# Kernel tuning notes

Hardware: AMD Instinct MI355X
Metric: run time of the kernel (lower is better)

## Reference

```python
import jax, jax.numpy as jnp
import numpy as np

B = 4
IMAGE = 64
SAMPLES = 24
LATENT = 128
HIDDEN = 128
CAMERA_D = 2.0
NEAR, FAR = CAMERA_D - 1.0, CAMERA_D + 1.0
FOV_T = float(np.tan(np.arcsin(1.0 / CAMERA_D)))  # frustum tangent to unit sphere
SHARPNESS = 50.0


def _view_field():
    # canonical per-pixel ray directions, camera looking down -z
    c = ((np.arange(IMAGE) + 0.5) / IMAGE * 2.0 - 1.0) * FOV_T
    xx, yy = np.meshgrid(c, -c, indexing='xy')  # [H, W]
    d = np.stack([xx, yy, -np.ones_like(xx)], axis=-1)
    d /= np.linalg.norm(d, axis=-1, keepdims=True)
    return d.astype(np.float32)  # [H, W, 3]


def _frustum_mask_idx():
    # static mask: pixels whose canonical ray intersects the unit sphere
    d = _view_field().reshape(-1, 3)
    o = np.array([0.0, 0.0, CAMERA_D])
    disc = (d @ o) ** 2 - (o @ o - 1.0)
    return np.nonzero(disc >= 0.0)[0].astype(np.int32)


def setup_inputs() -> dict:
    key = jax.random.key(0)
    k = jax.random.split(key, 8)

    def w(ki, shape):
        return jax.random.normal(ki, shape, jnp.float32) * np.sqrt(2.0 / shape[0])

    return {
        'latents': jax.random.normal(k[0], (B, LATENT), jnp.float32) * 0.01,
        'phis': jax.random.uniform(k[1], (B,), jnp.float32) * (np.pi / 3.0),
        'thetas': jax.random.uniform(k[2], (B,), jnp.float32) * (2.0 * np.pi),
        'samples_u': jax.random.uniform(k[3], (IMAGE, IMAGE, SAMPLES), jnp.float32),
        'w1': w(k[4], (3 + LATENT, HIDDEN)), 'b1': jnp.zeros((HIDDEN,), jnp.float32),
        'w2': w(k[5], (HIDDEN, HIDDEN)), 'b2': jnp.zeros((HIDDEN,), jnp.float32),
        'w_sdf': w(k[6], (HIDDEN, 1)), 'b_sdf': jnp.zeros((1,), jnp.float32),
        'w_tex': w(k[7], (HIDDEN, 3)), 'b_tex': jnp.zeros((3,), jnp.float32),
    }


def reference(latents, phis, thetas, samples_u, w1, b1, w2, b2, w_sdf, b_sdf, w_tex, b_tex):
    mask_idx = jnp.asarray(_frustum_mask_idx())  # [R] static
    n_rays = int(mask_idx.shape[0])
    d_cam = jnp.asarray(_view_field())  # [H, W, 3]

    def feats(P, Z):  # latent-conditioned SDF MLP trunk
        h = jax.nn.relu(jnp.concatenate([P, Z], -1) @ w1 + b1)
        return jax.nn.relu(h @ w2 + b2)

    def sdf_val(P, Z):
        return (feats(P, Z) @ w_sdf + b_sdf)[..., 0]

    # sphereToRect: camera position on sphere of radius CAMERA_D
    cp, sp = jnp.cos(phis), jnp.sin(phis)
    ct, st = jnp.cos(thetas), jnp.sin(thetas)
    cam_loc = CAMERA_D * jnp.stack([cp * st, sp, cp * ct], -1)  # [B, 3]

    # enumerateRays: rotate canonical view field to look at the origin
    f = -cam_loc / jnp.linalg.norm(cam_loc, axis=-1, keepdims=True)
    up0 = jnp.broadcast_to(jnp.array([0.0, 1.0, 0.0], jnp.float32), f.shape)
    right = jnp.cross(up0, f)
    right = right / jnp.linalg.norm(right, axis=-1, keepdims=True)
    up = jnp.cross(f, right)
    R = jnp.stack([right, up, -f], axis=-1)  # [B, 3, 3], columns = camera axes
    rays = jnp.einsum('bij,hwj->bhwi', R, d_cam).reshape(B, IMAGE * IMAGE, 3)
    rays_m = rays[:, mask_idx]  # [B, R, 3]

    # sampleStratified: per-pixel jittered depths in [NEAR, FAR]
    bins = (jnp.arange(SAMPLES, dtype=jnp.float32) + samples_u) * ((FAR - NEAR) / SAMPLES) + NEAR
    samples_m = bins.reshape(IMAGE * IMAGE, SAMPLES)[mask_idx]  # [R, S]

    # scaleRays: world-space sample points per ray
    targets = cam_loc[:, None, None, :] + rays_m[:, :, None, :] * samples_m[None, :, :, None]  # [B,R,S,3]

    # fastRayIntegral: SDF at all samples, pick first sub-zero crossing per ray
    Z_all = jnp.broadcast_to(latents[:, None, :], (B, n_rays * SAMPLES, LATENT)).reshape(-1, LATENT)
    vals = sdf_val(targets.reshape(-1, 3), Z_all).reshape(B, n_rays, SAMPLES)
    below = vals <= 0.0
    idx = jnp.where(below.any(-1), jnp.argmax(below, -1), jnp.argmin(vals, -1))  # [B, R]
    hit = jnp.take_along_axis(targets, idx[:, :, None, None], axis=2)[:, :, 0]  # [B, R, 3]
    Ph = hit.reshape(-1, 3)
    Zh = jnp.broadcast_to(latents[:, None, :], (B, n_rays, LATENT)).reshape(-1, LATENT)
    values, vjp = jax.vjp(lambda P: sdf_val(P, Zh), Ph)
    normals, = vjp(jnp.ones_like(values))  # SDF spatial gradient = surface normal
    texture = jax.nn.sigmoid(feats(Ph, Zh) @ w_tex + b_tex)  # [B*R, 3]

    # shade: Lambertian with soft hit weight, then masked scatter into the image
    light = jnp.array([1.0, 1.0, 1.0], jnp.float32) / np.sqrt(3.0)
    n_hat = normals / (jnp.linalg.norm(normals, axis=-1, keepdims=True) + 1e-8)
    lambert = jnp.clip(n_hat @ light, 0.0, 1.0)
    hit_w = jax.nn.sigmoid(-values * SHARPNESS)
    shaded = (texture * ((0.2 + 0.8 * lambert) * hit_w)[:, None]).reshape(B, n_rays, 3)
    result = jnp.zeros((B, IMAGE * IMAGE, 3), shaded.dtype).at[:, mask_idx].set(shaded)
    return result.reshape(B, IMAGE, IMAGE, 3).transpose(0, 3, 1, 2)  # [B, 3, H, W]
```

## Files before the change

### kernel.cpp

```cpp
#include <hip/hip_runtime.h>
#include <math.h>

typedef short bf16x8 __attribute__((ext_vector_type(8)));
typedef float f32x4 __attribute__((ext_vector_type(4)));

#define BATCH 4
#define IMG 64
#define NSAMP 24
#define HID 128
#define LATN 128
#define PIX 8
#define MPT (PIX*NSAMP)
#define FOV_T 0.57735026918962576f
#define CAMD 2.0f
#define NEARP 1.0f
#define STEP (2.0f/24.0f)
#define SHARP 50.0f

#define WS_LAT1 0
#define WS_CAMR 512
#define WS_W2T  1024
#define WS_L1P  17408
#define WS_W2S  19456

__device__ __forceinline__ unsigned short f2bf(float f) {
    unsigned int u = __float_as_uint(f);
    u = u + 0x7FFFu + ((u >> 16) & 1u);
    return (unsigned short)(u >> 16);
}
__device__ __forceinline__ float bf2f(unsigned short s) {
    return __uint_as_float(((unsigned int)s) << 16);
}

__global__ void setup_batch(const float* __restrict__ latents,
                            const float* __restrict__ phis,
                            const float* __restrict__ thetas,
                            const float* __restrict__ w1,
                            const float* __restrict__ b1,
                            float* __restrict__ ws) {
    int b = blockIdx.x, j = threadIdx.x;
    float acc = b1[j];
    for (int k = 0; k < LATN; ++k)
        acc = fmaf(latents[b*LATN + k], w1[(3+k)*HID + j], acc);
    ws[WS_LAT1 + b*HID + j] = acc;
    float4 pk = make_float4(w1[j], w1[HID + j], w1[2*HID + j], acc);
    *(float4*)&ws[WS_L1P + (b*HID + j)*4] = pk;
    if (j == 0) {
        float ph = phis[b], th = thetas[b];
        float cp = cosf(ph), sp = sinf(ph), ct = cosf(th), st = sinf(th);
        float cx = CAMD*cp*st, cy = CAMD*sp, cz = CAMD*cp*ct;
        float nc = sqrtf(cx*cx + cy*cy + cz*cz);
        float fx = -cx/nc, fy = -cy/nc, fz = -cz/nc;
        float rx = fz, rz = -fx;
        float nr = sqrtf(rx*rx + rz*rz);
        rx /= nr; rz /= nr;
        float ux = fy*rz;
        float uy = fz*rx - fx*rz;
        float uz = -fy*rx;
        float* c = ws + WS_CAMR + b*12;
        c[0]=cx; c[1]=cy; c[2]=cz;
        c[3]=rx; c[4]=0.0f; c[5]=rz;
        c[6]=ux; c[7]=uy; c[8]=uz;
        c[9]=fx; c[10]=fy; c[11]=fz;
    }
}

__global__ void setup_w2t(const float* __restrict__ w2, float* __restrict__ ws) {
    int j = blockIdx.x, k = threadIdx.x;
    ws[WS_W2T + j*HID + k] = w2[k*HID + j];
}

__global__ void setup_w2s(const float* __restrict__ w2, unsigned short* __restrict__ w2s) {
    int id = blockIdx.x*256 + threadIdx.x;
    int k0 = id >> 9, n0 = (id >> 6) & 7, l = id & 63;
    int n = n0*16 + (l & 15);
    #pragma unroll
    for (int i = 0; i < 8; ++i) {
        int k = k0*32 + (l >> 4)*8 + i;
        float w = w2[k*HID + n];
        unsigned short u0 = f2bf(w);   float f0 = bf2f(u0);
        float r1 = w - f0;  unsigned short u1 = f2bf(r1); float f1 = bf2f(u1);
        float r2 = r1 - f1; unsigned short u2 = f2bf(r2);
        int base = ((k0*8 + n0)*64 + l)*8 + i;
        w2s[base]         = u0;
        w2s[16384 + base] = u1;
        w2s[32768 + base] = u2;
    }
}

__global__ __launch_bounds__(256, 2)
void render_kernel(const float* __restrict__ samples_u,
                   const float* __restrict__ w1,
                   const float* __restrict__ w2,
                   const float* __restrict__ b2,
                   const float* __restrict__ w_sdf,
                   const float* __restrict__ b_sdf,
                   const float* __restrict__ w_tex,
                   const float* __restrict__ b_tex,
                   const float* __restrict__ ws,
                   float* __restrict__ out) {
    __shared__ __align__(16) float4 Ps4[MPT];
    __shared__ __align__(16) float4 l1ps[HID];
    __shared__ float vals[MPT];
    __shared__ float b2s[HID];
    __shared__ float wsds[HID];
    __shared__ float shadeH[4*HID];
    __shared__ float shadeD[4*HID];
    __shared__ float lat1s[HID];
    __shared__ float camR[12];
    __shared__ int   hitMs[PIX];
    __shared__ int   maskq[PIX];

    const int t    = threadIdx.x;
    const int lane = t & 63;
    const int wv   = __builtin_amdgcn_readfirstlane(t >> 6);
    const int blk  = blockIdx.x;
    const int b    = blk >> 9;
    const int tile = blk & 511;

    if (t < 12)  camR[t]  = ws[WS_CAMR + b*12 + t];
    if (t < HID) {
        lat1s[t] = ws[WS_LAT1 + b*HID + t];
        l1ps[t]  = ((const float4*)(ws + WS_L1P))[b*HID + t];
        b2s[t]   = b2[t];
        wsds[t]  = w_sdf[t];
    }
    if (t < PIX) {
        int p = tile*PIX + t;
        int x = p & 63, y = p >> 6;
        float xx = ((x + 0.5f)*(2.0f/IMG) - 1.0f)*FOV_T;
        float yy = ((y + 0.5f)*(2.0f/IMG) - 1.0f)*FOV_T;
        float n2 = xx*xx + yy*yy + 1.0f;
        maskq[t] = (4.0f - 3.0f*n2) >= 0.0f ? 1 : 0;
    }
    __syncthreads();

    {
        int any = maskq[0]|maskq[1]|maskq[2]|maskq[3]|maskq[4]|maskq[5]|maskq[6]|maskq[7];
        if (!any) {
            if (t < PIX*3) {
                int q = t & 7, ch = t >> 3;
                int p = tile*PIX + q;
                int x = p & 63, y = p >> 6;
                out[((b*3 + ch)*IMG + y)*IMG + x] = 0.0f;
            }
            return;
        }
    }

    if (t < MPT) {
        int q = t / NSAMP, s = t - q*NSAMP;
        int p = tile*PIX + q;
        int x = p & 63, y = p >> 6;
        float xx =  ((x + 0.5f)*(2.0f/IMG) - 1.0f)*FOV_T;
        float yy = -(((y + 0.5f)*(2.0f/IMG) - 1.0f)*FOV_T);
        float inv = 1.0f/sqrtf(xx*xx + yy*yy + 1.0f);
        float d0 = xx*inv, d1 = yy*inv, d2 = -inv;
        float rxv = camR[3]*d0 + camR[6]*d1 - camR[9]*d2;
        float ryv = camR[4]*d0 + camR[7]*d1 - camR[10]*d2;
        float rzv = camR[5]*d0 + camR[8]*d1 - camR[11]*d2;
        float u  = samples_u[(y*IMG + x)*NSAMP + s];
        float tv = (s + u)*STEP + NEARP;
        Ps4[t] = make_float4(fmaf(rxv, tv, camR[0]),
                             fmaf(ryv, tv, camR[1]),
                             fmaf(rzv, tv, camR[2]), 0.0f);
    }
    __syncthreads();

    {
        const unsigned short* w2s = (const unsigned short*)(ws + WS_W2S);
        const int lm = lane & 15, lg = lane >> 4;
        const float bsdf = b_sdf[0];

        float4 Pm0 = Ps4[(wv*3+0)*16 + lm];
        float4 Pm1 = Ps4[(wv*3+1)*16 + lm];
        float4 Pm2 = Ps4[(wv*3+2)*16 + lm];

        f32x4 acc[3][8];
        #pragma unroll
        for (int mt = 0; mt < 3; ++mt)
            #pragma unroll
            for (int n0 = 0; n0 < 8; ++n0)
                acc[mt][n0] = (f32x4)(0.0f);

        for (int k0 = 0; k0 < 4; ++k0) {
            bf16x8 a0[3], a1[3], a2[3];
            #pragma unroll
            for (int mt = 0; mt < 3; ++mt) {
                float4 P = (mt == 0) ? Pm0 : ((mt == 1) ? Pm1 : Pm2);
                #pragma unroll
                for (int i = 0; i < 8; ++i) {
                    float4 wl = l1ps[k0*32 + lg*8 + i];
                    float h = fmaxf(fmaf(P.x, wl.x, fmaf(P.y, wl.y, fmaf(P.z, wl.z, wl.w))), 0.0f);
                    unsigned short u0 = f2bf(h);  float f0 = bf2f(u0);
                    float r1 = h - f0;  unsigned short u1 = f2bf(r1); float f1 = bf2f(u1);
                    float r2 = r1 - f1; unsigned short u2 = f2bf(r2);
                    a0[mt][i] = (short)u0; a1[mt][i] = (short)u1; a2[mt][i] = (short)u2;
                }
            }
            const unsigned short* wk = w2s + (k0*8)*512 + lane*8;
            #pragma unroll
            for (int n0 = 0; n0 < 8; ++n0) {
                bf16x8 B0 = *(const bf16x8*)(wk + n0*512);
                bf16x8 B1 = *(const bf16x8*)(wk + 16384 + n0*512);
                bf16x8 B2 = *(const bf16x8*)(wk + 32768 + n0*512);
                #pragma unroll
                for (int mt = 0; mt < 3; ++mt) {
                    f32x4 c = acc[mt][n0];
                    c = __builtin_amdgcn_mfma_f32_16x16x32_bf16(a0[mt], B0, c, 0, 0, 0);
                    c = __builtin_amdgcn_mfma_f32_16x16x32_bf16(a0[mt], B1, c, 0, 0, 0);
                    c = __builtin_amdgcn_mfma_f32_16x16x32_bf16(a1[mt], B0, c, 0, 0, 0);
                    c = __builtin_amdgcn_mfma_f32_16x16x32_bf16(a0[mt], B2, c, 0, 0, 0);
                    c = __builtin_amdgcn_mfma_f32_16x16x32_bf16(a1[mt], B1, c, 0, 0, 0);
                    c = __builtin_amdgcn_mfma_f32_16x16x32_bf16(a2[mt], B0, c, 0, 0, 0);
                    acc[mt][n0] = c;
                }
            }
        }

        #pragma unroll
        for (int mt = 0; mt < 3; ++mt) {
            float ps0 = 0.0f, ps1 = 0.0f, ps2 = 0.0f, ps3 = 0.0f;
            #pragma unroll
            for (int n0 = 0; n0 < 8; ++n0) {
                int j = n0*16 + lm;
                float bb = b2s[j], wd = wsds[j];
                ps0 += fmaxf(acc[mt][n0][0] + bb, 0.0f)*wd;
                ps1 += fmaxf(acc[mt][n0][1] + bb, 0.0f)*wd;
                ps2 += fmaxf(acc[mt][n0][2] + bb, 0.0f)*wd;
                ps3 += fmaxf(acc[mt][n0][3] + bb, 0.0f)*wd;
            }
            #pragma unroll
            for (int off = 1; off < 16; off <<= 1) {
                ps0 += __shfl_xor(ps0, off, 64);
                ps1 += __shfl_xor(ps1, off, 64);
                ps2 += __shfl_xor(ps2, off, 64);
                ps3 += __shfl_xor(ps3, off, 64);
            }
            if (lm == 0) {
                int mg = (wv*3 + mt)*16 + lg*4;
                vals[mg+0] = ps0 + bsdf;
                vals[mg+1] = ps1 + bsdf;
                vals[mg+2] = ps2 + bsdf;
                vals[mg+3] = ps3 + bsdf;
            }
        }
    }
    __syncthreads();

    if (t < PIX) {
        int base = t*NSAMP;
        int idx = -1, bidx = 0;
        float bestv = 3.0e38f;
        for (int s = 0; s < NSAMP; ++s) {
            float v = vals[base + s];
            if (idx < 0 && v <= 0.0f) idx = s;
            if (v < bestv) { bestv = v; bidx = s; }
        }
        hitMs[t] = base + (idx >= 0 ? idx : bidx);
    }
    __syncthreads();

    const float* w2t = ws + WS_W2T;
    const int j0 = lane, j1 = lane + 64;

    for (int pp = 0; pp < 2; ++pp) {
        int pt = pp*4 + wv;
        int hm = hitMs[pt];
        float4 H = Ps4[hm];
        float hx = H.x, hy = H.y, hz = H.z;

        float z0 = fmaf(hx, w1[j0], fmaf(hy, w1[HID+j0], fmaf(hz, w1[2*HID+j0], lat1s[j0])));
        float z1 = fmaf(hx, w1[j1], fmaf(hy, w1[HID+j1], fmaf(hz, w1[2*HID+j1], lat1s[j1])));
        float h10 = fmaxf(z0, 0.0f), h11 = fmaxf(z1, 0.0f);
        shadeH[wv*HID + j0] = h10;
        shadeH[wv*HID + j1] = h11;

        float a00=0,a01=0,a02=0,a03=0, a10=0,a11=0,a12=0,a13=0;
        for (int k = 0; k < HID; k += 4) {
            float4 hv = *(const float4*)&shadeH[wv*HID + k];
            a00 = fmaf(hv.x, w2[(k+0)*HID + j0], a00);
            a10 = fmaf(hv.x, w2[(k+0)*HID + j1], a10);
            a01 = fmaf(hv.y, w2[(k+1)*HID + j0], a01);
            a11 = fmaf(hv.y, w2[(k+1)*HID + j1], a11);
            a02 = fmaf(hv.z, w2[(k+2)*HID + j0], a02);
            a12 = fmaf(hv.z, w2[(k+2)*HID + j1], a12);
            a03 = fmaf(hv.w, w2[(k+3)*HID + j0], a03);
            a13 = fmaf(hv.w, w2[(k+3)*HID + j1], a13);
        }
        float za = (a00+a01)+(a02+a03) + b2[j0];
        float zb = (a10+a11)+(a12+a13) + b2[j1];
        float h20 = fmaxf(za, 0.0f), h21 = fmaxf(zb, 0.0f);
        float wsd0 = w_sdf[j0], wsd1 = w_sdf[j1];
        shadeD[wv*HID + j0] = (za > 0.0f) ? wsd0 : 0.0f;
        shadeD[wv*HID + j1] = (zb > 0.0f) ? wsd1 : 0.0f;

        float pv = h20*wsd0 + h21*wsd1;
        float p0 = h20*w_tex[j0*3+0] + h21*w_tex[j1*3+0];
        float p1 = h20*w_tex[j0*3+1] + h21*w_tex[j1*3+1];
        float p2 = h20*w_tex[j0*3+2] + h21*w_tex[j1*3+2];
        #pragma unroll
        for (int off = 32; off > 0; off >>= 1) {
            pv += __shfl_xor(pv, off, 64);
            p0 += __shfl_xor(p0, off, 64);
            p1 += __shfl_xor(p1, off, 64);
            p2 += __shfl_xor(p2, off, 64);
        }

        float d00=0,d01=0,d02=0,d03=0, d10=0,d11=0,d12=0,d13=0;
        for (int k = 0; k < HID; k += 4) {
            float4 dv = *(const float4*)&shadeD[wv*HID + k];
            d00 = fmaf(dv.x, w2t[(k+0)*HID + j0], d00);
            d10 = fmaf(dv.x, w2t[(k+0)*HID + j1], d10);
            d01 = fmaf(dv.y, w2t[(k+1)*HID + j0], d01);
            d11 = fmaf(dv.y, w2t[(k+1)*HID + j1], d11);
            d02 = fmaf(dv.z, w2t[(k+2)*HID + j0], d02);
            d12 = fmaf(dv.z, w2t[(k+2)*HID + j1], d12);
            d03 = fmaf(dv.w, w2t[(k+3)*HID + j0], d03);
            d13 = fmaf(dv.w, w2t[(k+3)*HID + j1], d13);
        }
        float dh0 = (d00+d01)+(d02+d03);
        float dh1v = (d10+d11)+(d12+d13);
        float dz10 = (h10 > 0.0f) ? dh0 : 0.0f;
        float dz11 = (h11 > 0.0f) ? dh1v : 0.0f;
        float g0 = w1[j0]*dz10 + w1[j1]*dz11;
        float g1 = w1[HID+j0]*dz10 + w1[HID+j1]*dz11;
        float g2 = w1[2*HID+j0]*dz10 + w1[2*HID+j1]*dz11;
        #pragma unroll
        for (int off = 32; off > 0; off >>= 1) {
            g0 += __shfl_xor(g0, off, 64);
            g1 += __shfl_xor(g1, off, 64);
            g2 += __shfl_xor(g2, off, 64);
        }

        if (lane == 0) {
            float val = pv + b_sdf[0];
            float nn = sqrtf(g0*g0 + g1*g1 + g2*g2) + 1e-8f;
            const float is3 = 0.57735026918962576f;
            float lam = (g0 + g1 + g2)*is3/nn;
            lam = fminf(fmaxf(lam, 0.0f), 1.0f);
            float hw = 1.0f/(1.0f + expf(val*SHARP));
            float sh = (0.2f + 0.8f*lam)*hw;
            int p = tile*PIX + pt;
            int x = p & 63, y = p >> 6;
            float o0 = 0.0f, o1 = 0.0f, o2 = 0.0f;
            if (maskq[pt]) {
                o0 = sh/(1.0f + expf(-(p0 + b_tex[0])));
                o1 = sh/(1.0f + expf(-(p1 + b_tex[1])));
                o2 = sh/(1.0f + expf(-(p2 + b_tex[2])));
            }
            out[((b*3 + 0)*IMG + y)*IMG + x] = o0;
            out[((b*3 + 1)*IMG + y)*IMG + x] = o1;
            out[((b*3 + 2)*IMG + y)*IMG + x] = o2;
        }
    }
}

extern "C" void kernel_launch(void* const* d_in, const int* in_sizes, int n_in,
                              void* d_out, int out_size, void* d_ws, size_t ws_size,
                              hipStream_t stream) {
    const float* latents   = (const float*)d_in[0];
    const float* phis      = (const float*)d_in[1];
    const float* thetas    = (const float*)d_in[2];
    const float* samples_u = (const float*)d_in[3];
    const float* w1        = (const float*)d_in[4];
    const float* b1        = (const float*)d_in[5];
    const float* w2        = (const float*)d_in[6];
    const float* b2        = (const float*)d_in[7];
    const float* w_sdf     = (const float*)d_in[8];
    const float* b_sdf     = (const float*)d_in[9];
    const float* w_tex     = (const float*)d_in[10];
    const float* b_tex     = (const float*)d_in[11];
    float* out = (float*)d_out;
    float* ws  = (float*)d_ws;

    setup_batch<<<dim3(BATCH), dim3(HID), 0, stream>>>(latents, phis, thetas, w1, b1, ws);
    setup_w2t<<<dim3(HID), dim3(HID), 0, stream>>>(w2, ws);
    setup_w2s<<<dim3(8), dim3(256), 0, stream>>>(w2, (unsigned short*)(ws + WS_W2S));
    render_kernel<<<dim3(BATCH*(IMG*IMG/PIX)), dim3(256), 0, stream>>>(
        samples_u, w1, w2, b2, w_sdf, b_sdf, w_tex, b_tex, ws, out);
}
```

Baseline: 218.7 us.

## Batch hit-point shading across 8 pixels and merge setup kernels into one

The per-wave shading loop, which handled one pixel at a time with two hidden units per lane, becomes a block-wide pass. All 8 hit points go through layer 2 and its backward pass together, with each thread owning one hidden unit across 4 pixels, so each w2 weight load is reused four times. Partial sums are reduced through small shared arrays and finished by 8 threads. The three setup kernels are fused into one launch to cut launch overhead. The cost is extra barriers and shared memory, plus a serial epilogue on a few threads.

```diff
diff --git a/kernel.cpp b/kernel.cpp
--- a/kernel.cpp
+++ b/kernel.cpp
@@ -32,59 +32,63 @@
     return __uint_as_float(((unsigned int)s) << 16);
 }
 
-__global__ void setup_batch(const float* __restrict__ latents,
-                            const float* __restrict__ phis,
-                            const float* __restrict__ thetas,
-                            const float* __restrict__ w1,
-                            const float* __restrict__ b1,
-                            float* __restrict__ ws) {
-    int b = blockIdx.x, j = threadIdx.x;
-    float acc = b1[j];
-    for (int k = 0; k < LATN; ++k)
-        acc = fmaf(latents[b*LATN + k], w1[(3+k)*HID + j], acc);
-    ws[WS_LAT1 + b*HID + j] = acc;
-    float4 pk = make_float4(w1[j], w1[HID + j], w1[2*HID + j], acc);
-    *(float4*)&ws[WS_L1P + (b*HID + j)*4] = pk;
-    if (j == 0) {
-        float ph = phis[b], th = thetas[b];
-        float cp = cosf(ph), sp = sinf(ph), ct = cosf(th), st = sinf(th);
-        float cx = CAMD*cp*st, cy = CAMD*sp, cz = CAMD*cp*ct;
-        float nc = sqrtf(cx*cx + cy*cy + cz*cz);
-        float fx = -cx/nc, fy = -cy/nc, fz = -cz/nc;
-        float rx = fz, rz = -fx;
-        float nr = sqrtf(rx*rx + rz*rz);
-        rx /= nr; rz /= nr;
-        float ux = fy*rz;
-        float uy = fz*rx - fx*rz;
-        float uz = -fy*rx;
-        float* c = ws + WS_CAMR + b*12;
-        c[0]=cx; c[1]=cy; c[2]=cz;
-        c[3]=rx; c[4]=0.0f; c[5]=rz;
-        c[6]=ux; c[7]=uy; c[8]=uz;
-        c[9]=fx; c[10]=fy; c[11]=fz;
-    }
-}
-
-__global__ void setup_w2t(const float* __restrict__ w2, float* __restrict__ ws) {
-    int j = blockIdx.x, k = threadIdx.x;
-    ws[WS_W2T + j*HID + k] = w2[k*HID + j];
-}
-
-__global__ void setup_w2s(const float* __restrict__ w2, unsigned short* __restrict__ w2s) {
-    int id = blockIdx.x*256 + threadIdx.x;
-    int k0 = id >> 9, n0 = (id >> 6) & 7, l = id & 63;
-    int n = n0*16 + (l & 15);
-    #pragma unroll
-    for (int i = 0; i < 8; ++i) {
-        int k = k0*32 + (l >> 4)*8 + i;
-        float w = w2[k*HID + n];
-        unsigned short u0 = f2bf(w);   float f0 = bf2f(u0);
-        float r1 = w - f0;  unsigned short u1 = f2bf(r1); float f1 = bf2f(u1);
-        float r2 = r1 - f1; unsigned short u2 = f2bf(r2);
-        int base = ((k0*8 + n0)*64 + l)*8 + i;
-        w2s[base]         = u0;
-        w2s[16384 + base] = u1;
-        w2s[32768 + base] = u2;
+__global__ void setup_all(const float* __restrict__ latents,
+                          const float* __restrict__ phis,
+                          const float* __restrict__ thetas,
+                          const float* __restrict__ w1,
+                          const float* __restrict__ b1,
+                          const float* __restrict__ w2,
+                          float* __restrict__ ws) {
+    const int bid = blockIdx.x, t = threadIdx.x;
+    if (bid < 4) {
+        if (t < HID) {
+            int b = bid, j = t;
+            float acc = b1[j];
+            for (int k = 0; k < LATN; ++k)
+                acc = fmaf(latents[b*LATN + k], w1[(3+k)*HID + j], acc);
+            ws[WS_LAT1 + b*HID + j] = acc;
+            float4 pk = make_float4(w1[j], w1[HID + j], w1[2*HID + j], acc);
+            *(float4*)&ws[WS_L1P + (b*HID + j)*4] = pk;
+            if (j == 0) {
+                float ph = phis[b], th = thetas[b];
+                float cp = cosf(ph), sp = sinf(ph), ct = cosf(th), st = sinf(th);
+                float cx = CAMD*cp*st, cy = CAMD*sp, cz = CAMD*cp*ct;
+                float nc = sqrtf(cx*cx + cy*cy + cz*cz);
+                float fx = -cx/nc, fy = -cy/nc, fz = -cz/nc;
+                float rx = fz, rz = -fx;
+                float nr = sqrtf(rx*rx + rz*rz);
+                rx /= nr; rz /= nr;
+                float ux = fy*rz;
+                float uy = fz*rx - fx*rz;
+                float uz = -fy*rx;
+                float* c = ws + WS_CAMR + b*12;
+                c[0]=cx; c[1]=cy; c[2]=cz;
+                c[3]=rx; c[4]=0.0f; c[5]=rz;
+                c[6]=ux; c[7]=uy; c[8]=uz;
+                c[9]=fx; c[10]=fy; c[11]=fz;
+            }
+        }
+    } else if (bid < 68) {
+        int id = (bid - 4)*256 + t;
+        int j = id >> 7, k = id & 127;
+        ws[WS_W2T + j*HID + k] = w2[k*HID + j];
+    } else {
+        int id = (bid - 68)*256 + t;
+        unsigned short* w2s = (unsigned short*)(ws + WS_W2S);
+        int k0 = id >> 9, n0 = (id >> 6) & 7, l = id & 63;
+        int n = n0*16 + (l & 15);
+        #pragma unroll
+        for (int i = 0; i < 8; ++i) {
+            int k = k0*32 + (l >> 4)*8 + i;
+            float w = w2[k*HID + n];
+            unsigned short u0 = f2bf(w);   float f0 = bf2f(u0);
+            float r1 = w - f0;  unsigned short u1 = f2bf(r1); float f1 = bf2f(u1);
+            float r2 = r1 - f1; unsigned short u2 = f2bf(r2);
+            int base = ((k0*8 + n0)*64 + l)*8 + i;
+            w2s[base]         = u0;
+            w2s[16384 + base] = u1;
+            w2s[32768 + base] = u2;
+        }
     }
 }
 
@@ -101,13 +105,15 @@
                    float* __restrict__ out) {
     __shared__ __align__(16) float4 Ps4[MPT];
     __shared__ __align__(16) float4 l1ps[HID];
+    __shared__ __align__(16) float4 shadeHT[HID*2];
+    __shared__ __align__(16) float4 dz2s[HID*2];
     __shared__ float vals[MPT];
     __shared__ float b2s[HID];
     __shared__ float wsds[HID];
-    __shared__ float shadeH[4*HID];
-    __shared__ float shadeD[4*HID];
     __shared__ float lat1s[HID];
     __shared__ float camR[12];
+    __shared__ float redp[4][16];
+    __shared__ float redg[4][12];
     __shared__ int   hitMs[PIX];
     __shared__ int   maskq[PIX];
 
@@ -239,10 +245,10 @@
             }
             if (lm == 0) {
                 int mg = (wv*3 + mt)*16 + lg*4;
-                vals[mg+0] = ps0 + bsdf;
-                vals[mg+1] = ps1 + bsdf;
-                vals[mg+2] = ps2 + bsdf;
-                vals[mg+3] = ps3 + bsdf;
+                vals[mg+0] = ps0 + b_sdf[0];
+                vals[mg+1] = ps1 + b_sdf[0];
+                vals[mg+2] = ps2 + b_sdf[0];
+                vals[mg+3] = ps3 + b_sdf[0];
             }
         }
     }
@@ -261,98 +267,132 @@
     }
     __syncthreads();
 
-    const float* w2t = ws + WS_W2T;
-    const int j0 = lane, j1 = lane + 64;
-
-    for (int pp = 0; pp < 2; ++pp) {
-        int pt = pp*4 + wv;
-        int hm = hitMs[pt];
-        float4 H = Ps4[hm];
-        float hx = H.x, hy = H.y, hz = H.z;
-
-        float z0 = fmaf(hx, w1[j0], fmaf(hy, w1[HID+j0], fmaf(hz, w1[2*HID+j0], lat1s[j0])));
-        float z1 = fmaf(hx, w1[j1], fmaf(hy, w1[HID+j1], fmaf(hz, w1[2*HID+j1], lat1s[j1])));
-        float h10 = fmaxf(z0, 0.0f), h11 = fmaxf(z1, 0.0f);
-        shadeH[wv*HID + j0] = h10;
-        shadeH[wv*HID + j1] = h11;
-
-        float a00=0,a01=0,a02=0,a03=0, a10=0,a11=0,a12=0,a13=0;
-        for (int k = 0; k < HID; k += 4) {
-            float4 hv = *(const float4*)&shadeH[wv*HID + k];
-            a00 = fmaf(hv.x, w2[(k+0)*HID + j0], a00);
-            a10 = fmaf(hv.x, w2[(k+0)*HID + j1], a10);
-            a01 = fmaf(hv.y, w2[(k+1)*HID + j0], a01);
-            a11 = fmaf(hv.y, w2[(k+1)*HID + j1], a11);
-            a02 = fmaf(hv.z, w2[(k+2)*HID + j0], a02);
-            a12 = fmaf(hv.z, w2[(k+2)*HID + j1], a12);
-            a03 = fmaf(hv.w, w2[(k+3)*HID + j0], a03);
-            a13 = fmaf(hv.w, w2[(k+3)*HID + j1], a13);
-        }
-        float za = (a00+a01)+(a02+a03) + b2[j0];
-        float zb = (a10+a11)+(a12+a13) + b2[j1];
-        float h20 = fmaxf(za, 0.0f), h21 = fmaxf(zb, 0.0f);
-        float wsd0 = w_sdf[j0], wsd1 = w_sdf[j1];
-        shadeD[wv*HID + j0] = (za > 0.0f) ? wsd0 : 0.0f;
-        shadeD[wv*HID + j1] = (zb > 0.0f) ? wsd1 : 0.0f;
-
-        float pv = h20*wsd0 + h21*wsd1;
-        float p0 = h20*w_tex[j0*3+0] + h21*w_tex[j1*3+0];
-        float p1 = h20*w_tex[j0*3+1] + h21*w_tex[j1*3+1];
-        float p2 = h20*w_tex[j0*3+2] + h21*w_tex[j1*3+2];
-        #pragma unroll
-        for (int off = 32; off > 0; off >>= 1) {
-            pv += __shfl_xor(pv, off, 64);
-            p0 += __shfl_xor(p0, off, 64);
-            p1 += __shfl_xor(p1, off, 64);
-            p2 += __shfl_xor(p2, off, 64);
-        }
-
-        float d00=0,d01=0,d02=0,d03=0, d10=0,d11=0,d12=0,d13=0;
-        for (int k = 0; k < HID; k += 4) {
-            float4 dv = *(const float4*)&shadeD[wv*HID + k];
-            d00 = fmaf(dv.x, w2t[(k+0)*HID + j0], d00);
-            d10 = fmaf(dv.x, w2t[(k+0)*HID + j1], d10);
-            d01 = fmaf(dv.y, w2t[(k+1)*HID + j0], d01);
-            d11 = fmaf(dv.y, w2t[(k+1)*HID + j1], d11);
-            d02 = fmaf(dv.z, w2t[(k+2)*HID + j0], d02);
-            d12 = fmaf(dv.z, w2t[(k+2)*HID + j1], d12);
-            d03 = fmaf(dv.w, w2t[(k+3)*HID + j0], d03);
-            d13 = fmaf(dv.w, w2t[(k+3)*HID + j1], d13);
-        }
-        float dh0 = (d00+d01)+(d02+d03);
-        float dh1v = (d10+d11)+(d12+d13);
-        float dz10 = (h10 > 0.0f) ? dh0 : 0.0f;
-        float dz11 = (h11 > 0.0f) ? dh1v : 0.0f;
-        float g0 = w1[j0]*dz10 + w1[j1]*dz11;
-        float g1 = w1[HID+j0]*dz10 + w1[HID+j1]*dz11;
-        float g2 = w1[2*HID+j0]*dz10 + w1[2*HID+j1]*dz11;
-        #pragma unroll
-        for (int off = 32; off > 0; off >>= 1) {
-            g0 += __shfl_xor(g0, off, 64);
-            g1 += __shfl_xor(g1, off, 64);
-            g2 += __shfl_xor(g2, off, 64);
-        }
-
-        if (lane == 0) {
-            float val = pv + b_sdf[0];
-            float nn = sqrtf(g0*g0 + g1*g1 + g2*g2) + 1e-8f;
-            const float is3 = 0.57735026918962576f;
-            float lam = (g0 + g1 + g2)*is3/nn;
-            lam = fminf(fmaxf(lam, 0.0f), 1.0f);
-            float hw = 1.0f/(1.0f + expf(val*SHARP));
-            float sh = (0.2f + 0.8f*lam)*hw;
-            int p = tile*PIX + pt;
-            int x = p & 63, y = p >> 6;
-            float o0 = 0.0f, o1 = 0.0f, o2 = 0.0f;
-            if (maskq[pt]) {
-                o0 = sh/(1.0f + expf(-(p0 + b_tex[0])));
-                o1 = sh/(1.0f + expf(-(p1 + b_tex[1])));
-                o2 = sh/(1.0f + expf(-(p2 + b_tex[2])));
-            }
-            out[((b*3 + 0)*IMG + y)*IMG + x] = o0;
-            out[((b*3 + 1)*IMG + y)*IMG + x] = o1;
-            out[((b*3 + 2)*IMG + y)*IMG + x] = o2;
-        }
+
+    #pragma unroll
+    for (int i = 0; i < 4; ++i) {
+        int idx = i*256 + t;
+        int p = idx & 7, k = idx >> 3;
+        float4 wl = l1ps[k];
+        float4 P  = Ps4[hitMs[p]];
+        float h = fmaxf(fmaf(P.x, wl.x, fmaf(P.y, wl.y, fmaf(P.z, wl.z, wl.w))), 0.0f);
+        ((float*)shadeHT)[k*8 + p] = h;
+    }
+    __syncthreads();
+
+    {
+        const int j = t & 127, ph = t >> 7;
+        float ac0 = 0.0f, ac1 = 0.0f, ac2 = 0.0f, ac3 = 0.0f;
+        const float* w2col = w2 + j;
+        #pragma unroll 8
+        for (int k = 0; k < HID; ++k) {
+            float wv2 = w2col[k*HID];
+            float4 hk = shadeHT[k*2 + ph];
+            ac0 = fmaf(hk.x, wv2, ac0);
+            ac1 = fmaf(hk.y, wv2, ac1);
+            ac2 = fmaf(hk.z, wv2, ac2);
+            ac3 = fmaf(hk.w, wv2, ac3);
+        }
+        float b2j = b2s[j], wsdj = wsds[j];
+        float tx0 = w_tex[j*3+0], tx1 = w_tex[j*3+1], tx2 = w_tex[j*3+2];
+        float z[4] = {ac0 + b2j, ac1 + b2j, ac2 + b2j, ac3 + b2j};
+        float4 dzv;
+        float vp[4], tp0[4], tp1[4], tp2[4];
+        #pragma unroll
+        for (int pp = 0; pp < 4; ++pp) {
+            float h2 = fmaxf(z[pp], 0.0f);
+            ((float*)&dzv)[pp] = (z[pp] > 0.0f) ? wsdj : 0.0f;
+            vp[pp]  = h2*wsdj;
+            tp0[pp] = h2*tx0;
+            tp1[pp] = h2*tx1;
+            tp2[pp] = h2*tx2;
+        }
+        dz2s[j*2 + ph] = dzv;
+        #pragma unroll
+        for (int pp = 0; pp < 4; ++pp) {
+            float v = vp[pp], a = tp0[pp], bt = tp1[pp], c = tp2[pp];
+            #pragma unroll
+            for (int off = 32; off > 0; off >>= 1) {
+                v  += __shfl_xor(v,  off, 64);
+                a  += __shfl_xor(a,  off, 64);
+                bt += __shfl_xor(bt, off, 64);
+                c  += __shfl_xor(c,  off, 64);
+            }
+            if (lane == 0) {
+                redp[wv][pp*4+0] = v;
+                redp[wv][pp*4+1] = a;
+                redp[wv][pp*4+2] = bt;
+                redp[wv][pp*4+3] = c;
+            }
+        }
+    }
+    __syncthreads();
+
+    {
+        const int k = t & 127, ph = t >> 7;
+        float d0 = 0.0f, d1 = 0.0f, d2 = 0.0f, d3 = 0.0f;
+        const float* wtcol = ws + WS_W2T + k;
+        #pragma unroll 8
+        for (int j = 0; j < HID; ++j) {
+            float wt = wtcol[j*HID];
+            float4 dz = dz2s[j*2 + ph];
+            d0 = fmaf(dz.x, wt, d0);
+            d1 = fmaf(dz.y, wt, d1);
+            d2 = fmaf(dz.z, wt, d2);
+            d3 = fmaf(dz.w, wt, d3);
+        }
+        float4 hh = shadeHT[k*2 + ph];
+        float4 wl = l1ps[k];
+        float dzl[4] = { (hh.x > 0.0f) ? d0 : 0.0f,
+                         (hh.y > 0.0f) ? d1 : 0.0f,
+                         (hh.z > 0.0f) ? d2 : 0.0f,
+                         (hh.w > 0.0f) ? d3 : 0.0f };
+        #pragma unroll
+        for (int pp = 0; pp < 4; ++pp) {
+            float g0 = wl.x*dzl[pp];
+            float g1 = wl.y*dzl[pp];
+            float g2 = wl.z*dzl[pp];
+            #pragma unroll
+            for (int off = 32; off > 0; off >>= 1) {
+                g0 += __shfl_xor(g0, off, 64);
+                g1 += __shfl_xor(g1, off, 64);
+                g2 += __shfl_xor(g2, off, 64);
+            }
+            if (lane == 0) {
+                redg[wv][0*4+pp] = g0;
+                redg[wv][1*4+pp] = g1;
+                redg[wv][2*4+pp] = g2;
+            }
+        }
+    }
+    __syncthreads();
+
+    if (t < PIX) {
+        int p = t, pp = p & 3;
+        int wA = (p < 4) ? 0 : 2;
+        float val  = redp[wA][pp*4+0] + redp[wA+1][pp*4+0] + b_sdf[0];
+        float tex0 = redp[wA][pp*4+1] + redp[wA+1][pp*4+1] + b_tex[0];
+        float tex1 = redp[wA][pp*4+2] + redp[wA+1][pp*4+2] + b_tex[1];
+        float tex2 = redp[wA][pp*4+3] + redp[wA+1][pp*4+3] + b_tex[2];
+        float g0 = redg[wA][0*4+pp] + redg[wA+1][0*4+pp];
+        float g1 = redg[wA][1*4+pp] + redg[wA+1][1*4+pp];
+        float g2 = redg[wA][2*4+pp] + redg[wA+1][2*4+pp];
+        float nn = sqrtf(g0*g0 + g1*g1 + g2*g2) + 1e-8f;
+        const float is3 = 0.57735026918962576f;
+        float lam = (g0 + g1 + g2)*is3/nn;
+        lam = fminf(fmaxf(lam, 0.0f), 1.0f);
+        float hw = 1.0f/(1.0f + expf(val*SHARP));
+        float sh = (0.2f + 0.8f*lam)*hw;
+        int pg = tile*PIX + p;
+        int x = pg & 63, y = pg >> 6;
+        float o0 = 0.0f, o1 = 0.0f, o2 = 0.0f;
+        if (maskq[p]) {
+            o0 = sh/(1.0f + expf(-tex0));
+            o1 = sh/(1.0f + expf(-tex1));
+            o2 = sh/(1.0f + expf(-tex2));
+        }
+        out[((b*3 + 0)*IMG + y)*IMG + x] = o0;
+        out[((b*3 + 1)*IMG + y)*IMG + x] = o1;
+        out[((b*3 + 2)*IMG + y)*IMG + x] = o2;
     }
 }
 
@@ -374,9 +414,7 @@
     float* out = (float*)d_out;
     float* ws  = (float*)d_ws;
 
-    setup_batch<<<dim3(BATCH), dim3(HID), 0, stream>>>(latents, phis, thetas, w1, b1, ws);
-    setup_w2t<<<dim3(HID), dim3(HID), 0, stream>>>(w2, ws);
-    setup_w2s<<<dim3(8), dim3(256), 0, stream>>>(w2, (unsigned short*)(ws + WS_W2S));
+    setup_all<<<dim3(76), dim3(256), 0, stream>>>(latents, phis, thetas, w1, b1, w2, ws);
     render_kernel<<<dim3(BATCH*(IMG*IMG/PIX)), dim3(256), 0, stream>>>(
         samples_u, w1, w2, b2, w_sdf, b_sdf, w_tex, b_tex, ws, out);
 }
```

New measurement: 193.0 us. 1.13x faster.
